# Optimization experiments

Measured on AMD Instinct MI355X. Metric: run time of the kernel, lower is better.

## Reference

```python
import jax, jax.numpy as jnp
import numpy as np

N = 50000      # nodes
E = 800000     # edges (avg degree 16)
DIN = 128      # input_dim
DG = 128       # gnn_dim
DCLS = 128     # cls_dim
DOUT = 10      # output_dim
LMDA = 1.0     # rw_lmda
P_DROP = 0.5


def setup_inputs() -> dict:
    key = jax.random.key(0)
    ks = jax.random.split(key, 12)
    x = jax.random.normal(ks[0], (N, DIN), jnp.float32)
    edge_index = jax.random.randint(ks[1], (2, E), 0, N, dtype=jnp.int64)
    edge_weight = jax.random.uniform(ks[2], (E,), jnp.float32)
    def glorot(k, shape):
        lim = np.sqrt(6.0 / (shape[0] + shape[1])).astype(np.float32)
        return jax.random.uniform(k, shape, jnp.float32, -lim, lim)
    return dict(
        x=x, edge_index=edge_index, edge_weight=edge_weight,
        W_lin_in=glorot(ks[3], (DIN, DG)), b_lin_in=jnp.zeros((DG,), jnp.float32),
        W_agg_in=glorot(ks[4], (DG + DIN, DG)), b_agg_in=jnp.zeros((DG,), jnp.float32),
        W_lin_h=glorot(ks[5], (DG, DG)), b_lin_h=jnp.zeros((DG,), jnp.float32),
        W_agg_h=glorot(ks[6], (2 * DG, DG)), b_agg_h=jnp.zeros((DG,), jnp.float32),
        W_mlp1=glorot(ks[7], (DG, DCLS)), b_mlp1=jnp.zeros((DCLS,), jnp.float32),
        W_mlp2=glorot(ks[8], (DCLS, DOUT)), b_mlp2=jnp.zeros((DOUT,), jnp.float32),
    )


def _gs_layer(x, row, col, ew, inv_cnt, W_lin, b_lin, W_agg, b_agg):
    # GS_reweight: message = (1-lmda)*lin(x_j) + lmda*ew*lin(x_j), mean-aggregated
    # at row (flow='target_to_source': gather from col, scatter to row).
    h = x @ W_lin + b_lin                      # [N, DG] (lin before gather == lin(x_j))
    hj = h[col]                                # [E, DG] gather
    m = (1.0 - LMDA) * hj + LMDA * (ew[:, None] * hj)
    agg = jax.ops.segment_sum(m, row, num_segments=N) * inv_cnt[:, None]  # mean
    out = jnp.concatenate([agg, x], axis=-1) @ W_agg + b_agg              # update()
    return jax.nn.relu(out)


def _dropout(x, k):
    mask = jax.random.bernoulli(k, 1.0 - P_DROP, x.shape)
    return jnp.where(mask, x / (1.0 - P_DROP), 0.0)


def reference(x, edge_index, edge_weight,
              W_lin_in, b_lin_in, W_agg_in, b_agg_in,
              W_lin_h, b_lin_h, W_agg_h, b_agg_h,
              W_mlp1, b_mlp1, W_mlp2, b_mlp2):
    row, col = edge_index[0], edge_index[1]
    cnt = jax.ops.segment_sum(jnp.ones((E,), x.dtype), row, num_segments=N)
    inv_cnt = 1.0 / jnp.maximum(cnt, 1.0)     # scatter_mean: empty rows -> 0
    dk = jax.random.split(jax.random.key(42), 3)
    h = _gs_layer(x, row, col, edge_weight, inv_cnt, W_lin_in, b_lin_in, W_agg_in, b_agg_in)
    h = _dropout(jax.nn.relu(h), dk[0])       # relu is idempotent after update's relu
    for i in range(2):                        # layers 2,3 share prop_hidden weights
        h = _gs_layer(h, row, col, edge_weight, inv_cnt, W_lin_h, b_lin_h, W_agg_h, b_agg_h)
        h = _dropout(jax.nn.relu(h), dk[i + 1])
    y = jax.nn.relu(h @ W_mlp1 + b_mlp1) @ W_mlp2 + b_mlp2  # cls_layers=2, bn=False
    return (h, y)
```

## Files before the change

### kernel.cpp

```cpp
#include <hip/hip_runtime.h>
#include <cstdint>
#include <cstddef>


#define N_NODES 50000
#define N_EDGES 800000
#define DGN 128
#define DOUT 10
#define NELEM (N_NODES * DGN)
#define NMASKW (NELEM / 64)
#define NBINS 391
#define TILE 4096
#define BSTR 4096
#define NTILES ((N_EDGES + TILE - 1) / TILE)
#define GBF ((N_NODES + 63) / 64)
#define MK_BLOCKS 25000

#define XB_BLK 6250
#define HI_BLK NTILES
#define WC_BLK 128
#define TR_BLK 192
#define R0 XB_BLK
#define R1 (R0 + HI_BLK)
#define R2 (R1 + WC_BLK)
#define R3 (R2 + TR_BLK)
#define MEGA_BLOCKS (R3 + 1)

#define AB_BLOCKS ((N_NODES + 3) / 4)

typedef __attribute__((ext_vector_type(8))) short bf16x8;
typedef __attribute__((ext_vector_type(4))) float f32x4;

__host__ __device__ static inline unsigned short f2bf(float f) {
  union { float f; unsigned u; } c; c.f = f;
  unsigned u = c.u;
  return (unsigned short)((u + 0x7fffu + ((u >> 16) & 1u)) >> 16);
}
__device__ static inline float bflo(unsigned u) { return __uint_as_float(u << 16); }
__device__ static inline float bfhi(unsigned u) { return __uint_as_float(u & 0xffff0000u); }
__device__ static inline float bf2f(unsigned short h) {
  return __uint_as_float(((unsigned)h) << 16);
}

__host__ __device__ static inline void tf2x32(unsigned k0, unsigned k1,
                                              unsigned c0, unsigned c1,
                                              unsigned& o0, unsigned& o1) {
  unsigned ks2 = k0 ^ k1 ^ 0x1BD11BDAu;
  unsigned x0 = c0 + k0;
  unsigned x1 = c1 + k1;
#define TFR(r) { x0 += x1; x1 = (x1 << (r)) | (x1 >> (32 - (r))); x1 ^= x0; }
  TFR(13) TFR(15) TFR(26) TFR(6)
  x0 += k1;  x1 += ks2 + 1u;
  TFR(17) TFR(29) TFR(16) TFR(24)
  x0 += ks2; x1 += k0 + 2u;
  TFR(13) TFR(15) TFR(26) TFR(6)
  x0 += k0;  x1 += k1 + 3u;
  TFR(17) TFR(29) TFR(16) TFR(24)
  x0 += k1;  x1 += ks2 + 4u;
  TFR(13) TFR(15) TFR(26) TFR(6)
  x0 += ks2; x1 += k0 + 5u;
#undef TFR
  o0 = x0; o1 = x1;
}

__device__ static inline void mask_chunk(unsigned long long* __restrict__ gm,
                                         int i, unsigned k0, unsigned k1) {
  unsigned o0, o1;
  tf2x32(k0, k1, 0u, (unsigned)i, o0, o1);
  unsigned long long b = __ballot(((o0 ^ o1) >> 31) == 0u);
  if ((threadIdx.x & 63) == 0) gm[i >> 6] = b;
}

__global__ __launch_bounds__(256) void mega_kernel(
    const float* __restrict__ x, unsigned short* __restrict__ xb,
    const int* __restrict__ ei, int* __restrict__ chist,
    const float* __restrict__ Wli, const float* __restrict__ Wai,
    const float* __restrict__ Wlh, const float* __restrict__ Wah,
    const float* __restrict__ Wm1,
    const float* __restrict__ bli, const float* __restrict__ blh,
    unsigned short* __restrict__ Tai, unsigned short* __restrict__ Tah,
    unsigned short* __restrict__ Tm1,
    float* __restrict__ bvi, float* __restrict__ bvh) {
  __shared__ int h[NBINS];
  const int b = blockIdx.x;
  const int tid = threadIdx.x;

  if (b < R0) {
    int g = b * 256 + tid;
    float4 v = ((const float4*)x)[g];
    ushort4 o;
    o.x = f2bf(v.x); o.y = f2bf(v.y); o.z = f2bf(v.z); o.w = f2bf(v.w);
    ((ushort4*)xb)[g] = o;
  } else if (b < R1) {
    for (int i = tid; i < NBINS; i += 256) h[i] = 0;
    __syncthreads();
    const int e0 = (b - R0) * TILE;
#pragma unroll 4
    for (int j = 0; j < TILE; j += 256) {
      int e = e0 + j + tid;
      if (e < N_EDGES) {
        int r = ei[e];
        r = (r < 0) ? 0 : (r >= N_NODES ? N_NODES - 1 : r);
        atomicAdd(&h[r >> 7], 1);
      }
    }
    __syncthreads();
    for (int i = tid; i < NBINS; i += 256)
      if (h[i]) atomicAdd(&chist[i], h[i]);
  } else if (b < R2) {
    int idx = (b - R1) * 256 + tid;
    int n = idx & 127;
    int k = (idx >> 7) & 127;
    int m = idx >> 14;
    const float* Wl = m ? Wlh : Wli;
    const float* Wa = m ? Wah : Wai;
    unsigned short* T = m ? Tah : Tai;
    float acc = 0.0f;
#pragma unroll 8
    for (int j = 0; j < 128; ++j)
      acc += Wl[k * 128 + j] * Wa[j * 128 + n];
    T[n * 256 + k] = f2bf(acc);
  } else if (b < R3) {
    int j = (b - R2) * 256 + tid;
    if (j < 16384) {
      int kk = j & 127, n = j >> 7;
      Tai[n * 256 + 128 + kk] = f2bf(Wai[(size_t)(128 + kk) * 128 + n]);
    } else if (j < 32768) {
      int q = j - 16384;
      int kk = q & 127, n = q >> 7;
      Tah[n * 256 + 128 + kk] = f2bf(Wah[(size_t)(128 + kk) * 128 + n]);
    } else {
      int q = j - 32768;
      int k = q & 127, n = q >> 7;
      Tm1[n * 128 + k] = f2bf(Wm1[(size_t)k * 128 + n]);
    }
  } else {
    int n = tid & 127;
    const float* bl = (tid < 128) ? bli : blh;
    const float* Wa = (tid < 128) ? Wai : Wah;
    float acc = 0.0f;
    for (int j = 0; j < 128; ++j) acc += bl[j] * Wa[j * 128 + n];
    if (tid < 128) bvi[n] = acc; else bvh[n] = acc;
  }
}

__global__ __launch_bounds__(256) void scatter_kernel(const int* __restrict__ ei,
                                                      const float* __restrict__ ew,
                                                      int* __restrict__ ccursor,
                                                      uint2* __restrict__ pk,
                                                      unsigned long long* __restrict__ mg0,
                                                      unsigned k00, unsigned k01) {
  if (blockIdx.x >= NTILES) {
    mask_chunk(mg0, (blockIdx.x - NTILES) * 256 + threadIdx.x, k00, k01);
    return;
  }
  __shared__ uint2 st[TILE];
  __shared__ unsigned short sbin[TILE];
  __shared__ int h[NBINS];
  __shared__ int base[NBINS];
  __shared__ int gbase[NBINS];
  __shared__ int cur[NBINS];
  __shared__ int sc[512];
  const int tid = threadIdx.x;
  const int e0 = blockIdx.x * TILE;
  const int nt = (N_EDGES - e0 < TILE) ? (N_EDGES - e0) : TILE;

  for (int i = tid; i < NBINS; i += 256) { h[i] = 0; cur[i] = 0; }
  __syncthreads();
  for (int j = tid; j < nt; j += 256) {
    int r = ei[e0 + j];
    r = (r < 0) ? 0 : (r >= N_NODES ? N_NODES - 1 : r);
    atomicAdd(&h[r >> 7], 1);
  }
  __syncthreads();
  sc[tid] = (tid < NBINS) ? h[tid] : 0;
  sc[tid + 256] = (tid + 256 < NBINS) ? h[tid + 256] : 0;
  __syncthreads();
  for (int off = 1; off < 512; off <<= 1) {
    int a0 = (tid >= off) ? sc[tid - off] : 0;
    int a1 = (tid + 256 >= off) ? sc[tid + 256 - off] : 0;
    __syncthreads();
    sc[tid] += a0; sc[tid + 256] += a1;
    __syncthreads();
  }
  if (tid < NBINS) {
    base[tid] = sc[tid] - h[tid];
    if (h[tid]) gbase[tid] = tid * BSTR + atomicAdd(&ccursor[tid], h[tid]);
  }
  if (tid + 256 < NBINS) {
    base[tid + 256] = sc[tid + 256] - h[tid + 256];
    if (h[tid + 256])
      gbase[tid + 256] = (tid + 256) * BSTR + atomicAdd(&ccursor[tid + 256], h[tid + 256]);
  }
  __syncthreads();
  for (int j = tid; j < nt; j += 256) {
    int r = ei[e0 + j];
    r = (r < 0) ? 0 : (r >= N_NODES ? N_NODES - 1 : r);
    int c = ei[N_EDGES + e0 + j];
    c = (c < 0) ? 0 : (c >= N_NODES ? N_NODES - 1 : c);
    int bb = r >> 7;
    int slot = base[bb] + atomicAdd(&cur[bb], 1);
    uint2 p;
    p.x = ((unsigned)r << 16) | (unsigned)c;
    p.y = __float_as_uint(ew[e0 + j]);
    st[slot] = p;
    sbin[slot] = (unsigned short)bb;
  }
  __syncthreads();
  for (int j = tid; j < nt; j += 256) {
    int bb = sbin[j];
    pk[(size_t)gbase[bb] + (j - base[bb])] = st[j];
  }
}

__global__ __launch_bounds__(256) void place_kernel(const int* __restrict__ chist,
                                                    const uint2* __restrict__ pk,
                                                    uint2* __restrict__ csr,
                                                    int* __restrict__ rowptr,
                                                    float* __restrict__ invc) {
  __shared__ int red[256];
  __shared__ int lcnt[128];
  __shared__ int lpre[128];
  __shared__ int lcur[128];
  __shared__ int sc[128];
  const int b = blockIdx.x;
  const int tid = threadIdx.x;

  int psum = 0;
  for (int i = tid; i < b; i += 256) psum += chist[i];
  red[tid] = psum;
  __syncthreads();
  for (int off = 128; off > 0; off >>= 1) {
    if (tid < off) red[tid] += red[tid + off];
    __syncthreads();
  }
  const int cb = red[0];
  const int n = chist[b];
  const uint2* __restrict__ pkb = pk + (size_t)b * BSTR;
  const int r0 = b << 7;
  const int nr = (N_NODES - r0 < 128) ? (N_NODES - r0) : 128;

  if (tid < 128) { lcnt[tid] = 0; lcur[tid] = 0; }
  __syncthreads();
  for (int i = tid; i < n; i += 256) {
    int r7 = (int)(pkb[i].x >> 16) - r0;
    atomicAdd(&lcnt[r7], 1);
  }
  __syncthreads();
  if (tid < 128) sc[tid] = lcnt[tid];
  __syncthreads();
  for (int off = 1; off < 128; off <<= 1) {
    int tv = (tid >= off && tid < 128) ? sc[tid - off] : 0;
    __syncthreads();
    if (tid < 128) sc[tid] += tv;
    __syncthreads();
  }
  if (tid < 128) lpre[tid] = sc[tid] - lcnt[tid];
  __syncthreads();
  if (tid < nr) {
    rowptr[r0 + tid] = cb + lpre[tid];
    int c = lcnt[tid];
    invc[r0 + tid] = 1.0f / (float)(c > 1 ? c : 1);
  }
  if (b == NBINS - 1 && tid == 0) rowptr[N_NODES] = N_EDGES;
  for (int i = tid; i < n; i += 256) {
    uint2 p = pkb[i];
    int r7 = (int)(p.x >> 16) - r0;
    int slot = cb + lpre[r7] + atomicAdd(&lcur[r7], 1);
    uint2 o;
    o.x = p.x & 0xFFFFu;
    o.y = p.y;
    csr[slot] = o;
  }
}

__global__ __launch_bounds__(256) void agg_kernel(const unsigned short* __restrict__ hlin,
                                                  const int* __restrict__ rowptr,
                                                  const uint2* __restrict__ csr,
                                                  const float* __restrict__ invc,
                                                  unsigned short* __restrict__ agg,
                                                  float* __restrict__ swout) {
  const int r = blockIdx.x * 4 + (threadIdx.x >> 6);
  const int lane = threadIdx.x & 63;
  const int es = lane >> 4;
  const int cg = lane & 15;
  const int start = rowptr[r];
  const int num = rowptr[r + 1] - start;
  const uint4* __restrict__ H = (const uint4*)hlin;

  int qi = (num > 0) ? (start + (lane < num ? lane : num - 1)) : 0;
  uint2 myq = csr[qi];

  float a[8] = {0.f, 0.f, 0.f, 0.f, 0.f, 0.f, 0.f, 0.f};
  float ws = 0.f;
  const int nb = (num < 64) ? num : 64;
  for (int e = 0; e < nb; e += 16) {
#pragma unroll
    for (int j = 0; j < 4; ++j) {
      int idx = e + j * 4 + es;
      bool ok = idx < nb;
      int sl = ok ? idx : nb - 1;
      int c0 = __shfl((int)myq.x, sl);
      int w0 = __shfl((int)myq.y, sl);
      unsigned col = (unsigned)c0;
      float w = ok ? __uint_as_float((unsigned)w0) : 0.0f;
      uint4 p = H[(size_t)col * 16 + cg];
      ws += w;
      a[0] += w * bflo(p.x); a[1] += w * bfhi(p.x);
      a[2] += w * bflo(p.y); a[3] += w * bfhi(p.y);
      a[4] += w * bflo(p.z); a[5] += w * bfhi(p.z);
      a[6] += w * bflo(p.w); a[7] += w * bfhi(p.w);
    }
  }
  for (int e = 64; e < num; e += 16) {
#pragma unroll
    for (int j = 0; j < 4; ++j) {
      int idx = e + j * 4 + es;
      bool ok = idx < num;
      int idxc = ok ? idx : (num - 1);
      uint2 q = csr[start + idxc];
      float w = ok ? __uint_as_float(q.y) : 0.0f;
      uint4 p = H[(size_t)q.x * 16 + cg];
      ws += w;
      a[0] += w * bflo(p.x); a[1] += w * bfhi(p.x);
      a[2] += w * bflo(p.y); a[3] += w * bfhi(p.y);
      a[4] += w * bflo(p.z); a[5] += w * bfhi(p.z);
      a[6] += w * bflo(p.w); a[7] += w * bfhi(p.w);
    }
  }
#pragma unroll
  for (int k = 0; k < 8; ++k) {
    a[k] += __shfl_xor(a[k], 32);
    a[k] += __shfl_xor(a[k], 16);
  }
  ws += __shfl_xor(ws, 32);
  ws += __shfl_xor(ws, 16);
  const float s = invc[r];
  if (es == 0) {
    uint4 o;
    o.x = (unsigned)f2bf(a[0] * s) | ((unsigned)f2bf(a[1] * s) << 16);
    o.y = (unsigned)f2bf(a[2] * s) | ((unsigned)f2bf(a[3] * s) << 16);
    o.z = (unsigned)f2bf(a[4] * s) | ((unsigned)f2bf(a[5] * s) << 16);
    o.w = (unsigned)f2bf(a[6] * s) | ((unsigned)f2bf(a[7] * s) << 16);
    ((uint4*)agg)[(size_t)r * 16 + cg] = o;
  }
  if (swout && lane == 0) swout[r] = ws * s;
}

template <bool WF32, bool MASKGEN, bool MLP>
__global__ __launch_bounds__(256) void layer_gemm(
    const unsigned short* __restrict__ Agg, const unsigned short* __restrict__ Hin,
    const unsigned short* __restrict__ Wt,
    const float* __restrict__ bvec, const float* __restrict__ bagg,
    const float* __restrict__ sw,
    const unsigned long long* __restrict__ maskw,
    float* __restrict__ outf, unsigned short* __restrict__ outb,
    unsigned long long* __restrict__ gm, unsigned gk0, unsigned gk1,
    const unsigned short* __restrict__ Wt2,
    const float* __restrict__ b1,
    const float* __restrict__ W2, const float* __restrict__ b2,
    float* __restrict__ y) {
  if (MASKGEN && blockIdx.x >= GBF) {
    mask_chunk(gm, (blockIdx.x - GBF) * 256 + threadIdx.x, gk0, gk1);
    return;
  }
  constexpr int LS = 72;
  constexpr int LT = 132;
  __shared__ unsigned short Als[64 * LS];
  __shared__ unsigned short Bls[128 * LS];
  __shared__ unsigned short tT[MLP ? 64 * LT : 2];
  __shared__ float Ws[MLP ? 128 * DOUT : 1];
  __shared__ float bs[MLP ? DOUT : 1];
  const int tid = threadIdx.x;
  const int m0 = blockIdx.x * 64;
  const int lane = tid & 63;
  const int wid = tid >> 6;
  const int wm = (wid >> 1) * 32;
  const int wn = (wid & 1) * 64;
  const int ln = lane & 15;
  const int lh = lane >> 4;
  const int sArow = tid >> 2;
  const int sAk = (tid & 3) * 16;
  const int sBcol = tid >> 1;
  const int sBk = (tid & 1) * 32;
  int arow = m0 + sArow;
  if (arow >= N_NODES) arow = N_NODES - 1;

  if (MLP) {
    for (int i = tid; i < 128 * DOUT; i += 256) Ws[i] = W2[i];
    if (tid < DOUT) bs[tid] = b2[tid];
  }

  f32x4 acc[2][4];
#pragma unroll
  for (int i = 0; i < 2; ++i)
#pragma unroll
    for (int j = 0; j < 4; ++j)
#pragma unroll
      for (int r = 0; r < 4; ++r) acc[i][j][r] = 0.0f;

  for (int kb = 0; kb < 256; kb += 64) {
    const unsigned short* Asrc = (kb < 128) ? Agg : Hin;
    const unsigned short* ap = Asrc + (size_t)arow * 128 + (kb & 127) + sAk;
    unsigned short* al = &Als[sArow * LS + sAk];
    *(uint4*)(al + 0) = *(const uint4*)(ap + 0);
    *(uint4*)(al + 8) = *(const uint4*)(ap + 8);
    const unsigned short* bp = Wt + (size_t)sBcol * 256 + kb + sBk;
    unsigned short* bl = &Bls[sBcol * LS + sBk];
    *(uint4*)(bl + 0)  = *(const uint4*)(bp + 0);
    *(uint4*)(bl + 8)  = *(const uint4*)(bp + 8);
    *(uint4*)(bl + 16) = *(const uint4*)(bp + 16);
    *(uint4*)(bl + 24) = *(const uint4*)(bp + 24);
    __syncthreads();
#pragma unroll
    for (int ks = 0; ks < 64; ks += 32) {
      bf16x8 af[2], bfr[4];
#pragma unroll
      for (int i = 0; i < 2; ++i)
        af[i] = *(const bf16x8*)&Als[(wm + i * 16 + ln) * LS + ks + lh * 8];
#pragma unroll
      for (int j = 0; j < 4; ++j)
        bfr[j] = *(const bf16x8*)&Bls[(wn + j * 16 + ln) * LS + ks + lh * 8];
#pragma unroll
      for (int i = 0; i < 2; ++i)
#pragma unroll
        for (int j = 0; j < 4; ++j)
          acc[i][j] = __builtin_amdgcn_mfma_f32_16x16x32_bf16(af[i], bfr[j], acc[i][j], 0, 0, 0);
    }
    __syncthreads();
  }

  const int lm = lane >> 4;
  float bc[4], b2c[4];
#pragma unroll
  for (int j = 0; j < 4; ++j) {
    int col = wn + j * 16 + ln;
    bc[j] = bvec[col];
    b2c[j] = bagg[col];
  }
#pragma unroll
  for (int i = 0; i < 2; ++i) {
    const int lr0 = wm + i * 16 + lm * 4;
#pragma unroll
    for (int r = 0; r < 4; ++r) {
      const int row = m0 + lr0 + r;
      if (row >= N_NODES) continue;
      const float swr = sw[row];
      const unsigned long long mw = maskw[(size_t)row * 2 + (wn >> 6)];
#pragma unroll
      for (int j = 0; j < 4; ++j) {
        const int col = wn + j * 16 + ln;
        float v = acc[i][j][r] + swr * bc[j] + b2c[j];
        v = fmaxf(v, 0.0f);
        v = ((mw >> (col & 63)) & 1ull) ? 2.0f * v : 0.0f;
        if (WF32) outf[(size_t)row * DGN + col] = v;
        if (MLP) tT[(lr0 + r) * LT + col] = f2bf(v);
        else outb[(size_t)row * DGN + col] = f2bf(v);
      }
    }
  }

  if (MLP) {
    __syncthreads();

    f32x4 acc2[2][4];
#pragma unroll
    for (int i = 0; i < 2; ++i)
#pragma unroll
      for (int j = 0; j < 4; ++j)
#pragma unroll
        for (int r = 0; r < 4; ++r) acc2[i][j][r] = 0.0f;

    for (int kb = 0; kb < 128; kb += 64) {
      const unsigned short* bp = Wt2 + (size_t)sBcol * 128 + kb + sBk;
      unsigned short* bl = &Bls[sBcol * LS + sBk];
      *(uint4*)(bl + 0)  = *(const uint4*)(bp + 0);
      *(uint4*)(bl + 8)  = *(const uint4*)(bp + 8);
      *(uint4*)(bl + 16) = *(const uint4*)(bp + 16);
      *(uint4*)(bl + 24) = *(const uint4*)(bp + 24);
      __syncthreads();
#pragma unroll
      for (int ks = 0; ks < 64; ks += 32) {
        bf16x8 af[2], bfr[4];
#pragma unroll
        for (int i = 0; i < 2; ++i)
          af[i] = *(const bf16x8*)&tT[(wm + i * 16 + ln) * LT + kb + ks + lh * 8];
#pragma unroll
        for (int j = 0; j < 4; ++j)
          bfr[j] = *(const bf16x8*)&Bls[(wn + j * 16 + ln) * LS + ks + lh * 8];
#pragma unroll
        for (int i = 0; i < 2; ++i)
#pragma unroll
          for (int j = 0; j < 4; ++j)
            acc2[i][j] = __builtin_amdgcn_mfma_f32_16x16x32_bf16(af[i], bfr[j], acc2[i][j], 0, 0, 0);
      }
      __syncthreads();
    }

    float bcol[4];
#pragma unroll
    for (int j = 0; j < 4; ++j) bcol[j] = b1[wn + j * 16 + ln];
#pragma unroll
    for (int i = 0; i < 2; ++i) {
      const int lr0 = wm + i * 16 + lm * 4;
#pragma unroll
      for (int r = 0; r < 4; ++r) {
        const int lr = lr0 + r;
#pragma unroll
        for (int j = 0; j < 4; ++j) {
          const int col = wn + j * 16 + ln;
          float v = fmaxf(acc2[i][j][r] + bcol[j], 0.0f);
          tT[lr * LT + col] = f2bf(v);
        }
      }
    }
    __syncthreads();

    if (tid < 64) {
      int row = m0 + tid;
      if (row < N_NODES) {
        float a2[DOUT];
#pragma unroll
        for (int c = 0; c < DOUT; ++c) a2[c] = bs[c];
        const unsigned short* tr = &tT[tid * LT];
#pragma unroll 8
        for (int k = 0; k < 128; ++k) {
          float tv = bf2f(tr[k]);
          const float* wr = &Ws[k * DOUT];
#pragma unroll
          for (int c = 0; c < DOUT; ++c) a2[c] += tv * wr[c];
        }
        float* yp = y + (size_t)row * DOUT;
#pragma unroll
        for (int c = 0; c < DOUT; ++c) yp[c] = a2[c];
      }
    }
  }
}

extern "C" void kernel_launch(void* const* d_in, const int* in_sizes, int n_in,
                              void* d_out, int out_size, void* d_ws, size_t ws_size,
                              hipStream_t stream) {
  const float* x        = (const float*)d_in[0];
  const int*   ei       = (const int*)d_in[1];
  const float* ew       = (const float*)d_in[2];
  const float* W_lin_in = (const float*)d_in[3];
  const float* b_lin_in = (const float*)d_in[4];
  const float* W_agg_in = (const float*)d_in[5];
  const float* b_agg_in = (const float*)d_in[6];
  const float* W_lin_h  = (const float*)d_in[7];
  const float* b_lin_h  = (const float*)d_in[8];
  const float* W_agg_h  = (const float*)d_in[9];
  const float* b_agg_h  = (const float*)d_in[10];
  const float* W_mlp1   = (const float*)d_in[11];
  const float* b_mlp1   = (const float*)d_in[12];
  const float* W_mlp2   = (const float*)d_in[13];
  const float* b_mlp2   = (const float*)d_in[14];

  float* hout = (float*)d_out;
  float* yout = hout + (size_t)NELEM;

  char* p = (char*)d_ws;
  auto alloc = [&](size_t bytes) {
    char* q = p;
    p += (bytes + 255) & ~(size_t)255;
    return q;
  };
  int*   chist   = (int*)alloc((size_t)(NBINS + 1) * 4);
  int*   ccursor = (int*)alloc((size_t)NBINS * 4);
  int*   rowptr  = (int*)alloc((size_t)(N_NODES + 1) * 4);
  float* invc    = (float*)alloc((size_t)N_NODES * 4);
  float* swv     = (float*)alloc((size_t)N_NODES * 4);
  uint2* pk      = (uint2*)alloc((size_t)NBINS * BSTR * 8);
  uint2* csr     = (uint2*)alloc((size_t)N_EDGES * 8);
  unsigned short* xb   = (unsigned short*)alloc((size_t)NELEM * 2);
  unsigned short* aggb = (unsigned short*)alloc((size_t)NELEM * 2);
  unsigned short* hA   = (unsigned short*)alloc((size_t)NELEM * 2);
  unsigned short* hB   = (unsigned short*)alloc((size_t)NELEM * 2);
  unsigned long long* mw0 = (unsigned long long*)alloc((size_t)NMASKW * 8);
  unsigned long long* mw1 = (unsigned long long*)alloc((size_t)NMASKW * 8);
  unsigned long long* mw2 = (unsigned long long*)alloc((size_t)NMASKW * 8);
  unsigned short* Tai = (unsigned short*)alloc(32768 * 2);
  unsigned short* Tah = (unsigned short*)alloc(32768 * 2);
  unsigned short* Tm1 = (unsigned short*)alloc(16384 * 2);
  float* bvi = (float*)alloc(128 * 4);
  float* bvh = (float*)alloc(128 * 4);

  unsigned dk[3][2];
  for (unsigned i = 0; i < 3; ++i) tf2x32(0u, 42u, 0u, i, dk[i][0], dk[i][1]);

  hipMemsetAsync(chist, 0, (size_t)(NBINS + 1) * 4, stream);
  hipMemsetAsync(ccursor, 0, (size_t)NBINS * 4, stream);
  mega_kernel<<<MEGA_BLOCKS, 256, 0, stream>>>(
      x, xb, ei, chist, W_lin_in, W_agg_in, W_lin_h, W_agg_h, W_mlp1,
      b_lin_in, b_lin_h, Tai, Tah, Tm1, bvi, bvh);

  scatter_kernel<<<NTILES + MK_BLOCKS, 256, 0, stream>>>(
      ei, ew, ccursor, pk, mw0, dk[0][0], dk[0][1]);
  place_kernel<<<NBINS, 256, 0, stream>>>(chist, pk, csr, rowptr, invc);

  agg_kernel<<<AB_BLOCKS, 256, 0, stream>>>(xb, rowptr, csr, invc, aggb, swv);
  layer_gemm<false, true, false><<<GBF + MK_BLOCKS, 256, 0, stream>>>(
      aggb, xb, Tai, bvi, b_agg_in, swv, mw0, nullptr, hA,
      mw1, dk[1][0], dk[1][1], nullptr, nullptr, nullptr, nullptr, nullptr);

  agg_kernel<<<AB_BLOCKS, 256, 0, stream>>>(hA, rowptr, csr, invc, aggb, nullptr);
  layer_gemm<false, true, false><<<GBF + MK_BLOCKS, 256, 0, stream>>>(
      aggb, hA, Tah, bvh, b_agg_h, swv, mw1, nullptr, hB,
      mw2, dk[2][0], dk[2][1], nullptr, nullptr, nullptr, nullptr, nullptr);

  agg_kernel<<<AB_BLOCKS, 256, 0, stream>>>(hB, rowptr, csr, invc, aggb, nullptr);
  layer_gemm<true, false, true><<<GBF, 256, 0, stream>>>(
      aggb, hB, Tah, bvh, b_agg_h, swv, mw2, hout, nullptr,
      nullptr, 0, 0, Tm1, b_mlp1, W_mlp2, b_mlp2, yout);
}
```

Baseline: 310.0 us.

## Use 128-row GEMM tiles with 512 threads and MFMA for final projection

The layer GEMM kernel now processes 128 rows per block using 512 threads (8 waves), so the loaded weight tile is reused across twice as many rows and fewer blocks are launched. The final 128x10 output projection, previously a scalar loop run by 64 threads, now uses a bf16 MFMA with the W2 weights transposed and padded to 16 columns in shared memory. The extra mask-generation blocks are resized to match the 512-thread block. Risks: the larger per-block shared memory footprint may lower occupancy, and W2 is now rounded to bf16, which changes precision.

```diff
diff --git a/kernel.cpp b/kernel.cpp
--- a/kernel.cpp
+++ b/kernel.cpp
@@ -13,8 +13,9 @@
 #define TILE 4096
 #define BSTR 4096
 #define NTILES ((N_EDGES + TILE - 1) / TILE)
-#define GBF ((N_NODES + 63) / 64)
+#define GB128 ((N_NODES + 127) / 128)
 #define MK_BLOCKS 25000
+#define MKB512 12500
 
 #define XB_BLK 6250
 #define HI_BLK NTILES
@@ -38,9 +39,6 @@
 }
 __device__ static inline float bflo(unsigned u) { return __uint_as_float(u << 16); }
 __device__ static inline float bfhi(unsigned u) { return __uint_as_float(u & 0xffff0000u); }
-__device__ static inline float bf2f(unsigned short h) {
-  return __uint_as_float(((unsigned)h) << 16);
-}
 
 __host__ __device__ static inline void tf2x32(unsigned k0, unsigned k1,
                                               unsigned c0, unsigned c1,
@@ -348,7 +346,7 @@
 }
 
 template <bool WF32, bool MASKGEN, bool MLP>
-__global__ __launch_bounds__(256) void layer_gemm(
+__global__ __launch_bounds__(512) void layer_gemm(
     const unsigned short* __restrict__ Agg, const unsigned short* __restrict__ Hin,
     const unsigned short* __restrict__ Wt,
     const float* __restrict__ bvec, const float* __restrict__ bagg,
@@ -360,19 +358,19 @@
     const float* __restrict__ b1,
     const float* __restrict__ W2, const float* __restrict__ b2,
     float* __restrict__ y) {
-  if (MASKGEN && blockIdx.x >= GBF) {
-    mask_chunk(gm, (blockIdx.x - GBF) * 256 + threadIdx.x, gk0, gk1);
+  if (MASKGEN && blockIdx.x >= GB128) {
+    mask_chunk(gm, (blockIdx.x - GB128) * 512 + threadIdx.x, gk0, gk1);
     return;
   }
   constexpr int LS = 72;
   constexpr int LT = 132;
-  __shared__ unsigned short Als[64 * LS];
+  __shared__ unsigned short Als[128 * LS];
   __shared__ unsigned short Bls[128 * LS];
-  __shared__ unsigned short tT[MLP ? 64 * LT : 2];
-  __shared__ float Ws[MLP ? 128 * DOUT : 1];
+  __shared__ unsigned short tT[MLP ? 128 * LT : 2];
+  __shared__ unsigned short Wsb[MLP ? 16 * LT : 2];
   __shared__ float bs[MLP ? DOUT : 1];
   const int tid = threadIdx.x;
-  const int m0 = blockIdx.x * 64;
+  const int m0 = blockIdx.x * 128;
   const int lane = tid & 63;
   const int wid = tid >> 6;
   const int wm = (wid >> 1) * 32;
@@ -381,13 +379,14 @@
   const int lh = lane >> 4;
   const int sArow = tid >> 2;
   const int sAk = (tid & 3) * 16;
-  const int sBcol = tid >> 1;
-  const int sBk = (tid & 1) * 32;
   int arow = m0 + sArow;
   if (arow >= N_NODES) arow = N_NODES - 1;
 
   if (MLP) {
-    for (int i = tid; i < 128 * DOUT; i += 256) Ws[i] = W2[i];
+    for (int i = tid; i < 16 * 128; i += 512) {
+      int c = i >> 7, k = i & 127;
+      Wsb[c * LT + k] = (c < DOUT) ? f2bf(W2[(size_t)k * DOUT + c]) : (unsigned short)0;
+    }
     if (tid < DOUT) bs[tid] = b2[tid];
   }
 
@@ -405,12 +404,10 @@
     unsigned short* al = &Als[sArow * LS + sAk];
     *(uint4*)(al + 0) = *(const uint4*)(ap + 0);
     *(uint4*)(al + 8) = *(const uint4*)(ap + 8);
-    const unsigned short* bp = Wt + (size_t)sBcol * 256 + kb + sBk;
-    unsigned short* bl = &Bls[sBcol * LS + sBk];
-    *(uint4*)(bl + 0)  = *(const uint4*)(bp + 0);
-    *(uint4*)(bl + 8)  = *(const uint4*)(bp + 8);
-    *(uint4*)(bl + 16) = *(const uint4*)(bp + 16);
-    *(uint4*)(bl + 24) = *(const uint4*)(bp + 24);
+    const unsigned short* bp = Wt + (size_t)sArow * 256 + kb + sAk;
+    unsigned short* bl = &Bls[sArow * LS + sAk];
+    *(uint4*)(bl + 0) = *(const uint4*)(bp + 0);
+    *(uint4*)(bl + 8) = *(const uint4*)(bp + 8);
     __syncthreads();
 #pragma unroll
     for (int ks = 0; ks < 64; ks += 32) {
@@ -472,12 +469,10 @@
         for (int r = 0; r < 4; ++r) acc2[i][j][r] = 0.0f;
 
     for (int kb = 0; kb < 128; kb += 64) {
-      const unsigned short* bp = Wt2 + (size_t)sBcol * 128 + kb + sBk;
-      unsigned short* bl = &Bls[sBcol * LS + sBk];
-      *(uint4*)(bl + 0)  = *(const uint4*)(bp + 0);
-      *(uint4*)(bl + 8)  = *(const uint4*)(bp + 8);
-      *(uint4*)(bl + 16) = *(const uint4*)(bp + 16);
-      *(uint4*)(bl + 24) = *(const uint4*)(bp + 24);
+      const unsigned short* bp = Wt2 + (size_t)sArow * 128 + kb + sAk;
+      unsigned short* bl = &Bls[sArow * LS + sAk];
+      *(uint4*)(bl + 0) = *(const uint4*)(bp + 0);
+      *(uint4*)(bl + 8) = *(const uint4*)(bp + 8);
       __syncthreads();
 #pragma unroll
       for (int ks = 0; ks < 64; ks += 32) {
@@ -516,23 +511,20 @@
     }
     __syncthreads();
 
-    if (tid < 64) {
-      int row = m0 + tid;
-      if (row < N_NODES) {
-        float a2[DOUT];
-#pragma unroll
-        for (int c = 0; c < DOUT; ++c) a2[c] = bs[c];
-        const unsigned short* tr = &tT[tid * LT];
-#pragma unroll 8
-        for (int k = 0; k < 128; ++k) {
-          float tv = bf2f(tr[k]);
-          const float* wr = &Ws[k * DOUT];
-#pragma unroll
-          for (int c = 0; c < DOUT; ++c) a2[c] += tv * wr[c];
-        }
-        float* yp = y + (size_t)row * DOUT;
-#pragma unroll
-        for (int c = 0; c < DOUT; ++c) yp[c] = a2[c];
+    f32x4 acc3;
+#pragma unroll
+    for (int r = 0; r < 4; ++r) acc3[r] = 0.0f;
+#pragma unroll
+    for (int kt = 0; kt < 4; ++kt) {
+      bf16x8 af = *(const bf16x8*)&tT[(wid * 16 + ln) * LT + kt * 32 + lh * 8];
+      bf16x8 bw = *(const bf16x8*)&Wsb[ln * LT + kt * 32 + lh * 8];
+      acc3 = __builtin_amdgcn_mfma_f32_16x16x32_bf16(af, bw, acc3, 0, 0, 0);
+    }
+    if (ln < DOUT) {
+#pragma unroll
+      for (int r = 0; r < 4; ++r) {
+        const int row = m0 + wid * 16 + lm * 4 + r;
+        if (row < N_NODES) y[(size_t)row * DOUT + ln] = acc3[r] + bs[ln];
       }
     }
   }
@@ -600,17 +592,17 @@
   place_kernel<<<NBINS, 256, 0, stream>>>(chist, pk, csr, rowptr, invc);
 
   agg_kernel<<<AB_BLOCKS, 256, 0, stream>>>(xb, rowptr, csr, invc, aggb, swv);
-  layer_gemm<false, true, false><<<GBF + MK_BLOCKS, 256, 0, stream>>>(
+  layer_gemm<false, true, false><<<GB128 + MKB512, 512, 0, stream>>>(
       aggb, xb, Tai, bvi, b_agg_in, swv, mw0, nullptr, hA,
       mw1, dk[1][0], dk[1][1], nullptr, nullptr, nullptr, nullptr, nullptr);
 
   agg_kernel<<<AB_BLOCKS, 256, 0, stream>>>(hA, rowptr, csr, invc, aggb, nullptr);
-  layer_gemm<false, true, false><<<GBF + MK_BLOCKS, 256, 0, stream>>>(
+  layer_gemm<false, true, false><<<GB128 + MKB512, 512, 0, stream>>>(
       aggb, hA, Tah, bvh, b_agg_h, swv, mw1, nullptr, hB,
       mw2, dk[2][0], dk[2][1], nullptr, nullptr, nullptr, nullptr, nullptr);
 
   agg_kernel<<<AB_BLOCKS, 256, 0, stream>>>(hB, rowptr, csr, invc, aggb, nullptr);
-  layer_gemm<true, false, true><<<GBF, 256, 0, stream>>>(
+  layer_gemm<true, false, true><<<GB128, 512, 0, stream>>>(
       aggb, hB, Tah, bvh, b_agg_h, swv, mw2, hout, nullptr,
       nullptr, 0, 0, Tm1, b_mlp1, W_mlp2, b_mlp2, yout);
 }
```

Result: faster. 295.8 us (-4.6%).
